# Optimization experiments

Hardware: AMD Instinct MI355X
Metric: run time of the kernel (lower is better)

## Reference

```python
import jax, jax.numpy as jnp
import numpy as np

NEG_SLOPE = 0.01  # F.leaky_relu default
EPS = 1e-6


def setup_inputs() -> dict:
    key = jax.random.key(0)
    k1, k2, k3, k4 = jax.random.split(key, 4)
    N, E, IN, OUT = 100000, 1600000, 128, 64
    x = jax.random.normal(k1, (N, IN), dtype=jnp.float32)
    W = jax.random.normal(k2, (OUT, IN), dtype=jnp.float32) * (1.0 / np.sqrt(IN))
    a = jax.random.uniform(k3, (2 * OUT,), dtype=jnp.float32)  # uniform [0,1) as in init
    edge_index = jax.random.randint(k4, (2, E), 0, N, dtype=jnp.int64)
    return {"x": x, "W": W, "a": a, "edge_index": edge_index}


def reference(x, W, a, edge_index):
    N = x.shape[0]
    out_f = W.shape[0]
    # add self loops: append (i, i) for every node
    loops = jnp.arange(N, dtype=edge_index.dtype)
    ei = jnp.concatenate([edge_index, jnp.stack([loops, loops])], axis=1)
    src, dst = ei[0], ei[1]

    messages = x @ W.T                      # [N, out]
    h_src = messages[src]                   # [E', out]
    h_dst = messages[dst]                   # [E', out]

    # e = cat([h_dst, h_src]) . a  == h_dst.a[:out] + h_src.a[out:]
    e = h_dst @ a[:out_f] + h_src @ a[out_f:]
    e = jnp.where(e >= 0, e, NEG_SLOPE * e)  # leaky_relu
    w = jnp.exp(e)                           # unnormalized edge weights

    denom = jax.ops.segment_sum(w, dst, num_segments=N)                     # [N]
    agg = jax.ops.segment_sum(h_src * w[:, None], dst, num_segments=N)      # [N, out]
    return agg / jnp.clip(denom, EPS)[:, None]
```

## Files before the change

### kernel.cpp

```cpp
#include <hip/hip_runtime.h>
#include <hip/hip_bf16.h>

#define IN_F 128
#define OUT_F 64
#define NEG 0.01f

#define BUCKET_N 256
#define EPB 8192
#define CAP 48
#define MAXB 512
#define MAXSLAB 512
#define CMAXIT 32

__device__ __forceinline__ float leaky_exp(float e) {
    e = (e >= 0.f) ? e : NEG * e;
    return expf(e);
}

__device__ __forceinline__ float b2f(unsigned int v) { return __uint_as_float(v); }

__global__ __launch_bounds__(256) void wt_kernel(
    const float* __restrict__ W, float* __restrict__ Wtg)
{
    int i = blockIdx.x * 256 + threadIdx.x;
    int o = i >> 7, k = i & 127;
    Wtg[k * OUT_F + o] = W[i];
}

__global__ __launch_bounds__(256) void gemm_msg_kernel(
    const float* __restrict__ x, const float* __restrict__ Wtg,
    const float* __restrict__ a,
    __hip_bfloat16* __restrict__ msg, float2* __restrict__ ab, int N)
{
    const int tid = threadIdx.x;
    const int base = blockIdx.x * 64;
    const int tx = tid & 15;
    const int ty = tid >> 4;

    const float4* xr[4];
#pragma unroll
    for (int ri = 0; ri < 4; ++ri) {
        int row = min(base + ty * 4 + ri, N - 1);
        xr[ri] = (const float4*)x + (size_t)row * (IN_F / 4);
    }

    float4 xc[4];
#pragma unroll
    for (int ri = 0; ri < 4; ++ri) xc[ri] = xr[ri][0];

    const float4* wt4 = (const float4*)Wtg;

    float acc[4][4] = {};
#pragma unroll 2
    for (int k4 = 0; k4 < IN_F / 4; ++k4) {
        float4 xn[4];
        const int kn = min(k4 + 1, IN_F / 4 - 1);
#pragma unroll
        for (int ri = 0; ri < 4; ++ri) xn[ri] = xr[ri][kn];

        float wq[4][4];
#pragma unroll
        for (int j = 0; j < 4; ++j)
            *(float4*)wq[j] = wt4[(k4 * 4 + j) * (OUT_F / 4) + tx];
        float xq[4][4];
#pragma unroll
        for (int ri = 0; ri < 4; ++ri) *(float4*)xq[ri] = xc[ri];

#pragma unroll
        for (int ri = 0; ri < 4; ++ri)
#pragma unroll
            for (int ci = 0; ci < 4; ++ci) {
                acc[ri][ci] += xq[ri][0] * wq[0][ci];
                acc[ri][ci] += xq[ri][1] * wq[1][ci];
                acc[ri][ci] += xq[ri][2] * wq[2][ci];
                acc[ri][ci] += xq[ri][3] * wq[3][ci];
            }
#pragma unroll
        for (int ri = 0; ri < 4; ++ri) xc[ri] = xn[ri];
    }

    float a_lo[4], a_hi[4];
#pragma unroll
    for (int ci = 0; ci < 4; ++ci) {
        a_lo[ci] = a[tx * 4 + ci];
        a_hi[ci] = a[OUT_F + tx * 4 + ci];
    }

#pragma unroll
    for (int ri = 0; ri < 4; ++ri) {
        int row = base + ty * 4 + ri;
        if (row < N) {
            union { ushort4 u; __hip_bfloat16 h[4]; } pk;
            pk.h[0] = __float2bfloat16(acc[ri][0]);
            pk.h[1] = __float2bfloat16(acc[ri][1]);
            pk.h[2] = __float2bfloat16(acc[ri][2]);
            pk.h[3] = __float2bfloat16(acc[ri][3]);
            *(ushort4*)&msg[(size_t)row * OUT_F + tx * 4] = pk.u;
        }
        float pa = acc[ri][0] * a_lo[0] + acc[ri][1] * a_lo[1] +
                   acc[ri][2] * a_lo[2] + acc[ri][3] * a_lo[3];
        float pb = acc[ri][0] * a_hi[0] + acc[ri][1] * a_hi[1] +
                   acc[ri][2] * a_hi[2] + acc[ri][3] * a_hi[3];
#pragma unroll
        for (int off = 1; off < 16; off <<= 1) {
            pa += __shfl_xor(pa, off);
            pb += __shfl_xor(pb, off);
        }
        if (tx == 0 && row < N) ab[row] = make_float2(pa, pb);
    }
}

__global__ __launch_bounds__(512) void partition_kernel(
    const int* __restrict__ src, const int* __restrict__ dst,
    int* __restrict__ counts, unsigned int* __restrict__ cells,
    int* __restrict__ bucket_tot, int E, int B, int NBLKP)
{
    __shared__ int cnt_s[MAXB];
    for (int i = threadIdx.x; i < B; i += 512) cnt_s[i] = 0;
    __syncthreads();

    const size_t pbase = (size_t)blockIdx.x * B;

#pragma unroll
    for (int u = 0; u < 4; ++u) {
        const int i4 = blockIdx.x * 2048 + u * 512 + threadIdx.x;
        const int e0 = i4 * 4;
        if (e0 + 3 < E) {
            int4 s4 = ((const int4*)src)[i4];
            int4 d4 = ((const int4*)dst)[i4];
            int b0 = d4.x >> 8, b1 = d4.y >> 8, b2 = d4.z >> 8, b3 = d4.w >> 8;
            int r0 = atomicAdd(&cnt_s[b0], 1);
            int r1 = atomicAdd(&cnt_s[b1], 1);
            int r2 = atomicAdd(&cnt_s[b2], 1);
            int r3 = atomicAdd(&cnt_s[b3], 1);
            if (r0 < CAP) cells[(pbase + b0) * CAP + r0] =
                (unsigned)s4.x | ((unsigned)(d4.x & 255) << 20);
            if (r1 < CAP) cells[(pbase + b1) * CAP + r1] =
                (unsigned)s4.y | ((unsigned)(d4.y & 255) << 20);
            if (r2 < CAP) cells[(pbase + b2) * CAP + r2] =
                (unsigned)s4.z | ((unsigned)(d4.z & 255) << 20);
            if (r3 < CAP) cells[(pbase + b3) * CAP + r3] =
                (unsigned)s4.w | ((unsigned)(d4.w & 255) << 20);
        } else {
            for (int e = e0; e < E && e < e0 + 4; ++e) {
                int s = src[e], d = dst[e];
                int b = d >> 8;
                int r = atomicAdd(&cnt_s[b], 1);
                if (r < CAP) cells[(pbase + b) * CAP + r] =
                    (unsigned)s | ((unsigned)(d & 255) << 20);
            }
        }
    }
    __syncthreads();
    for (int i = threadIdx.x; i < B; i += 512) {
        int c = min(cnt_s[i], CAP);
        counts[(size_t)i * NBLKP + blockIdx.x] = c;
        atomicAdd(&bucket_tot[i], c);
    }
}

__global__ __launch_bounds__(512) void bucket_scan_kernel(
    const int* __restrict__ bucket_tot, int* __restrict__ bucket_base,
    int* __restrict__ offs, int N, int B)
{
    __shared__ int tmp[512];
    const int t = threadIdx.x;
    int v = 0;
    if (t < B) {
        int nodes = N - t * BUCKET_N;
        nodes = max(0, min(BUCKET_N, nodes));
        v = bucket_tot[t] + nodes;
    }
    tmp[t] = v;
    __syncthreads();
#pragma unroll
    for (int d = 1; d < 512; d <<= 1) {
        int add = (t >= d) ? tmp[t - d] : 0;
        __syncthreads();
        tmp[t] += add;
        __syncthreads();
    }
    if (t < B) bucket_base[t] = tmp[t] - v;
    if (t == 511) offs[N] = tmp[511];
}

__global__ __launch_bounds__(512) void compact_kernel(
    const int* __restrict__ counts, const unsigned int* __restrict__ cells,
    const int* __restrict__ bucket_base, const float2* __restrict__ ab,
    int* __restrict__ offs, int2* __restrict__ edges,
    int N, int B, int NBLK, int NBLKP)
{
    __shared__ int cnt_l[MAXSLAB];
    __shared__ int hist[BUCKET_N];
    __shared__ int scan_s[BUCKET_N];
    __shared__ int cursor[BUCKET_N];
    __shared__ float alpha_s[BUCKET_N];
    const int b = blockIdx.x;
    const int tid = threadIdx.x;
    const int wave = tid >> 6, lane = tid & 63;

    for (int i = tid; i < NBLK; i += 512) cnt_l[i] = counts[(size_t)b * NBLKP + i];
    float2 myab = make_float2(0.f, 0.f);
    if (tid < BUCKET_N) {
        int g = b * BUCKET_N + tid;
        bool valid = (g < N);
        hist[tid] = valid ? 1 : 0;
        if (valid) myab = ab[g];
        alpha_s[tid] = myab.x;
    }
    __syncthreads();

    unsigned cell_c[CMAXIT];
#pragma unroll
    for (int it = 0; it < CMAXIT; ++it) {
        int sl = wave + it * 8;
        unsigned v = 0xFFFFFFFFu;
        if (sl < NBLK) {
            int c = cnt_l[sl];
            if (lane < c) {
                v = cells[((size_t)sl * B + b) * CAP + lane];
                atomicAdd(&hist[v >> 20], 1);
            }
        }
        cell_c[it] = v;
    }
    for (int sl = wave + CMAXIT * 8; sl < NBLK; sl += 8) {
        int c = cnt_l[sl];
        if (lane < c) {
            unsigned v = cells[((size_t)sl * B + b) * CAP + lane];
            atomicAdd(&hist[v >> 20], 1);
        }
    }
    __syncthreads();

    int hv = 0;
    if (tid < BUCKET_N) { hv = hist[tid]; scan_s[tid] = hv; }
    __syncthreads();
#pragma unroll
    for (int d = 1; d < BUCKET_N; d <<= 1) {
        int add = (tid < BUCKET_N && tid >= d) ? scan_s[tid - d] : 0;
        __syncthreads();
        if (tid < BUCKET_N) scan_s[tid] += add;
        __syncthreads();
    }
    const int gbase = bucket_base[b];
    if (tid < BUCKET_N) {
        int excl = scan_s[tid] - hv;
        int g = b * BUCKET_N + tid;
        if (g < N) {
            offs[g] = gbase + excl;
            float wself = leaky_exp(myab.x + myab.y);
            edges[gbase + excl] = make_int2(g, __float_as_int(wself));
            cursor[tid] = excl + 1;
        }
    }
    __syncthreads();

#pragma unroll
    for (int it = 0; it < CMAXIT; ++it) {
        unsigned v = cell_c[it];
        if (v != 0xFFFFFFFFu) {
            int s = v & 0xFFFFF;
            int l = (v >> 20) & 255;
            float w = leaky_exp(alpha_s[l] + ab[s].y);
            int pos = atomicAdd(&cursor[l], 1);
            edges[gbase + pos] = make_int2(s, __float_as_int(w));
        }
    }
    for (int sl = wave + CMAXIT * 8; sl < NBLK; sl += 8) {
        int c = cnt_l[sl];
        if (lane < c) {
            unsigned v = cells[((size_t)sl * B + b) * CAP + lane];
            int s = v & 0xFFFFF;
            int l = (v >> 20) & 255;
            float w = leaky_exp(alpha_s[l] + ab[s].y);
            int pos = atomicAdd(&cursor[l], 1);
            edges[gbase + pos] = make_int2(s, __float_as_int(w));
        }
    }
}

__global__ __launch_bounds__(256) void aggregate_kernel(
    const int* __restrict__ offs, const int2* __restrict__ edges,
    const __hip_bfloat16* __restrict__ msg,
    float* __restrict__ out, int N)
{
    const int tid = threadIdx.x;
    const int node = blockIdx.x * 8 + (tid >> 5);
    if (node >= N) return;
    const int half = tid & 31;
    const int g = half & 7;
    const int u = half >> 3;

    const unsigned int* msp32 = (const unsigned int*)msg;

    float acc[8] = {0.f, 0.f, 0.f, 0.f, 0.f, 0.f, 0.f, 0.f};
    float den = 0.f;

    const int st = offs[node], en = offs[node + 1];
    const int deg = en - st;

    int idx = st + u;
    int j = 0;
    for (; j + 16 <= deg; j += 16) {
#pragma unroll
        for (int q = 0; q < 4; ++q) {
            int2 e = edges[idx + q * 4];
            float w = __int_as_float(e.y);
            uint4 m = *(const uint4*)&msp32[(size_t)e.x * (OUT_F / 2) + 4 * g];
            acc[0] += w * b2f(m.x << 16);
            acc[1] += w * b2f(m.x & 0xFFFF0000u);
            acc[2] += w * b2f(m.y << 16);
            acc[3] += w * b2f(m.y & 0xFFFF0000u);
            acc[4] += w * b2f(m.z << 16);
            acc[5] += w * b2f(m.z & 0xFFFF0000u);
            acc[6] += w * b2f(m.w << 16);
            acc[7] += w * b2f(m.w & 0xFFFF0000u);
            den += w;
        }
        idx += 16;
    }
    for (; j < deg; j += 4) {
        int ii = min(idx, en - 1);
        int2 e = edges[ii];
        float w = (idx < en) ? __int_as_float(e.y) : 0.f;
        uint4 m = *(const uint4*)&msp32[(size_t)e.x * (OUT_F / 2) + 4 * g];
        acc[0] += w * b2f(m.x << 16);
        acc[1] += w * b2f(m.x & 0xFFFF0000u);
        acc[2] += w * b2f(m.y << 16);
        acc[3] += w * b2f(m.y & 0xFFFF0000u);
        acc[4] += w * b2f(m.z << 16);
        acc[5] += w * b2f(m.z & 0xFFFF0000u);
        acc[6] += w * b2f(m.w << 16);
        acc[7] += w * b2f(m.w & 0xFFFF0000u);
        den += w;
        idx += 4;
    }

#pragma unroll
    for (int off = 8; off <= 16; off <<= 1) {
#pragma unroll
        for (int i = 0; i < 8; ++i) acc[i] += __shfl_xor(acc[i], off);
        den += __shfl_xor(den, off);
    }

    if (u == 0) {
        float dn = 1.f / fmaxf(den, 1e-6f);
        float4* op = (float4*)&out[(size_t)node * OUT_F + 8 * g];
        op[0] = make_float4(acc[0] * dn, acc[1] * dn, acc[2] * dn, acc[3] * dn);
        op[1] = make_float4(acc[4] * dn, acc[5] * dn, acc[6] * dn, acc[7] * dn);
    }
}

extern "C" void kernel_launch(void* const* d_in, const int* in_sizes, int n_in,
                              void* d_out, int out_size, void* d_ws, size_t ws_size,
                              hipStream_t stream) {
    const float* x  = (const float*)d_in[0];
    const float* W  = (const float*)d_in[1];
    const float* a  = (const float*)d_in[2];
    const int*   ei = (const int*)d_in[3];
    float* out = (float*)d_out;

    const int IN = in_sizes[1] / OUT_F;
    const int N  = in_sizes[0] / IN;
    const int E  = in_sizes[3] / 2;
    const int B  = (N + BUCKET_N - 1) / BUCKET_N;
    const int NBLK  = (E + EPB - 1) / EPB;
    const int NBLKP = (NBLK + 3) & ~3;

    auto align16 = [](size_t v) { return (v + 15) & ~(size_t)15; };
    char* p = (char*)d_ws;
    float* Wtg    = (float*)p; p += align16((size_t)IN_F * OUT_F * 4);
    __hip_bfloat16* msg = (__hip_bfloat16*)p; p += align16((size_t)N * OUT_F * 2);
    float2* ab    = (float2*)p; p += align16((size_t)N * 8);
    int*   counts = (int*)p;   p += align16((size_t)B * NBLKP * 4);
    unsigned int* cells = (unsigned int*)p; p += align16((size_t)NBLK * B * CAP * 4);
    int*   btot   = (int*)p;   p += align16((size_t)B * 4);
    int*   bbase  = (int*)p;   p += align16((size_t)B * 4);
    int*   offs   = (int*)p;   p += align16((size_t)(N + 1) * 4);
    int2*  edges  = (int2*)p;  p += align16((size_t)(E + N) * 8);

    const int* esrc = ei;
    const int* edst = ei + E;

    hipMemsetAsync(btot, 0, (size_t)B * 4, stream);

    wt_kernel<<<(IN_F * OUT_F) / 256, 256, 0, stream>>>(W, Wtg);
    gemm_msg_kernel<<<(N + 63) / 64, 256, 0, stream>>>(x, Wtg, a, msg, ab, N);
    partition_kernel<<<NBLK, 512, 0, stream>>>(esrc, edst, counts, cells,
                                               btot, E, B, NBLKP);
    bucket_scan_kernel<<<1, 512, 0, stream>>>(btot, bbase, offs, N, B);
    compact_kernel<<<B, 512, 0, stream>>>(counts, cells, bbase, ab,
                                          offs, edges, N, B, NBLK, NBLKP);
    aggregate_kernel<<<(N + 7) / 8, 256, 0, stream>>>(offs, edges, msg, out, N);
}
```

Measured before the change: 152.7 us.

## Hold W rows in registers, process one node per wave in GEMM

The GEMM is rewritten so that each lane keeps one full row of W (128 floats) in registers. Each wave then walks a contiguous range of nodes, and every lane produces one output feature per node. The x row is loaded uniformly across the wave, so it acts as a broadcast load. The attention dot products are now reduced with a 64-lane shuffle. The separate W transpose kernel and its workspace are removed. The cost is heavy register pressure (over 128 VGPRs per lane), which lowers occupancy, and a fixed grid of 1024 blocks with about 25 rows per wave.

After: 226.9 us. +48.6%, slower.

```diff
diff --git a/kernel.cpp b/kernel.cpp
--- a/kernel.cpp
+++ b/kernel.cpp
@@ -19,94 +19,63 @@
 
 __device__ __forceinline__ float b2f(unsigned int v) { return __uint_as_float(v); }
 
-__global__ __launch_bounds__(256) void wt_kernel(
-    const float* __restrict__ W, float* __restrict__ Wtg)
-{
-    int i = blockIdx.x * 256 + threadIdx.x;
-    int o = i >> 7, k = i & 127;
-    Wtg[k * OUT_F + o] = W[i];
-}
-
 __global__ __launch_bounds__(256) void gemm_msg_kernel(
-    const float* __restrict__ x, const float* __restrict__ Wtg,
+    const float* __restrict__ x, const float* __restrict__ W,
     const float* __restrict__ a,
-    __hip_bfloat16* __restrict__ msg, float2* __restrict__ ab, int N)
-{
-    const int tid = threadIdx.x;
-    const int base = blockIdx.x * 64;
-    const int tx = tid & 15;
-    const int ty = tid >> 4;
-
-    const float4* xr[4];
-#pragma unroll
-    for (int ri = 0; ri < 4; ++ri) {
-        int row = min(base + ty * 4 + ri, N - 1);
-        xr[ri] = (const float4*)x + (size_t)row * (IN_F / 4);
-    }
-
-    float4 xc[4];
-#pragma unroll
-    for (int ri = 0; ri < 4; ++ri) xc[ri] = xr[ri][0];
-
-    const float4* wt4 = (const float4*)Wtg;
-
-    float acc[4][4] = {};
-#pragma unroll 2
+    __hip_bfloat16* __restrict__ msg, float2* __restrict__ ab,
+    int N, int nwaves)
+{
+    const int lane = threadIdx.x & 63;
+
+    float w[IN_F];
+    const float4* wrow = (const float4*)(W + (size_t)lane * IN_F);
+#pragma unroll
     for (int k4 = 0; k4 < IN_F / 4; ++k4) {
-        float4 xn[4];
-        const int kn = min(k4 + 1, IN_F / 4 - 1);
-#pragma unroll
-        for (int ri = 0; ri < 4; ++ri) xn[ri] = xr[ri][kn];
-
-        float wq[4][4];
-#pragma unroll
-        for (int j = 0; j < 4; ++j)
-            *(float4*)wq[j] = wt4[(k4 * 4 + j) * (OUT_F / 4) + tx];
-        float xq[4][4];
-#pragma unroll
-        for (int ri = 0; ri < 4; ++ri) *(float4*)xq[ri] = xc[ri];
-
-#pragma unroll
-        for (int ri = 0; ri < 4; ++ri)
-#pragma unroll
-            for (int ci = 0; ci < 4; ++ci) {
-                acc[ri][ci] += xq[ri][0] * wq[0][ci];
-                acc[ri][ci] += xq[ri][1] * wq[1][ci];
-                acc[ri][ci] += xq[ri][2] * wq[2][ci];
-                acc[ri][ci] += xq[ri][3] * wq[3][ci];
-            }
-#pragma unroll
-        for (int ri = 0; ri < 4; ++ri) xc[ri] = xn[ri];
-    }
-
-    float a_lo[4], a_hi[4];
-#pragma unroll
-    for (int ci = 0; ci < 4; ++ci) {
-        a_lo[ci] = a[tx * 4 + ci];
-        a_hi[ci] = a[OUT_F + tx * 4 + ci];
-    }
-
-#pragma unroll
-    for (int ri = 0; ri < 4; ++ri) {
-        int row = base + ty * 4 + ri;
-        if (row < N) {
-            union { ushort4 u; __hip_bfloat16 h[4]; } pk;
-            pk.h[0] = __float2bfloat16(acc[ri][0]);
-            pk.h[1] = __float2bfloat16(acc[ri][1]);
-            pk.h[2] = __float2bfloat16(acc[ri][2]);
-            pk.h[3] = __float2bfloat16(acc[ri][3]);
-            *(ushort4*)&msg[(size_t)row * OUT_F + tx * 4] = pk.u;
-        }
-        float pa = acc[ri][0] * a_lo[0] + acc[ri][1] * a_lo[1] +
-                   acc[ri][2] * a_lo[2] + acc[ri][3] * a_lo[3];
-        float pb = acc[ri][0] * a_hi[0] + acc[ri][1] * a_hi[1] +
-                   acc[ri][2] * a_hi[2] + acc[ri][3] * a_hi[3];
-#pragma unroll
-        for (int off = 1; off < 16; off <<= 1) {
+        float4 wv = wrow[k4];
+        w[4 * k4 + 0] = wv.x;
+        w[4 * k4 + 1] = wv.y;
+        w[4 * k4 + 2] = wv.z;
+        w[4 * k4 + 3] = wv.w;
+    }
+    const float a_lo = a[lane];
+    const float a_hi = a[OUT_F + lane];
+
+    const int wid = __builtin_amdgcn_readfirstlane(
+        blockIdx.x * (blockDim.x >> 6) + (threadIdx.x >> 6));
+    const int rpw = (N + nwaves - 1) / nwaves;
+    const int r0 = wid * rpw;
+    const int r1 = min(r0 + rpw, N);
+
+    for (int row = r0; row < r1; ++row) {
+        const float4* xrow = (const float4*)(x + (size_t)row * IN_F);
+        float av0 = 0.f, av1 = 0.f, av2 = 0.f, av3 = 0.f;
+#pragma unroll
+        for (int k4 = 0; k4 < IN_F / 4; k4 += 4) {
+            float4 x0 = xrow[k4 + 0];
+            float4 x1 = xrow[k4 + 1];
+            float4 x2 = xrow[k4 + 2];
+            float4 x3 = xrow[k4 + 3];
+            av0 += x0.x * w[4 * k4 + 0] + x0.y * w[4 * k4 + 1]
+                 + x0.z * w[4 * k4 + 2] + x0.w * w[4 * k4 + 3];
+            av1 += x1.x * w[4 * k4 + 4] + x1.y * w[4 * k4 + 5]
+                 + x1.z * w[4 * k4 + 6] + x1.w * w[4 * k4 + 7];
+            av2 += x2.x * w[4 * k4 + 8] + x2.y * w[4 * k4 + 9]
+                 + x2.z * w[4 * k4 + 10] + x2.w * w[4 * k4 + 11];
+            av3 += x3.x * w[4 * k4 + 12] + x3.y * w[4 * k4 + 13]
+                 + x3.z * w[4 * k4 + 14] + x3.w * w[4 * k4 + 15];
+        }
+        const float acc = (av0 + av1) + (av2 + av3);
+
+        msg[(size_t)row * OUT_F + lane] = __float2bfloat16(acc);
+
+        float pa = acc * a_lo;
+        float pb = acc * a_hi;
+#pragma unroll
+        for (int off = 1; off < 64; off <<= 1) {
             pa += __shfl_xor(pa, off);
             pb += __shfl_xor(pb, off);
         }
-        if (tx == 0 && row < N) ab[row] = make_float2(pa, pb);
+        if (lane == 0) ab[row] = make_float2(pa, pb);
     }
 }
 
@@ -370,7 +339,6 @@
 
     auto align16 = [](size_t v) { return (v + 15) & ~(size_t)15; };
     char* p = (char*)d_ws;
-    float* Wtg    = (float*)p; p += align16((size_t)IN_F * OUT_F * 4);
     __hip_bfloat16* msg = (__hip_bfloat16*)p; p += align16((size_t)N * OUT_F * 2);
     float2* ab    = (float2*)p; p += align16((size_t)N * 8);
     int*   counts = (int*)p;   p += align16((size_t)B * NBLKP * 4);
@@ -385,8 +353,9 @@
 
     hipMemsetAsync(btot, 0, (size_t)B * 4, stream);
 
-    wt_kernel<<<(IN_F * OUT_F) / 256, 256, 0, stream>>>(W, Wtg);
-    gemm_msg_kernel<<<(N + 63) / 64, 256, 0, stream>>>(x, Wtg, a, msg, ab, N);
+    const int gemm_blocks = 1024;
+    const int nwaves = gemm_blocks * 4;
+    gemm_msg_kernel<<<gemm_blocks, 256, 0, stream>>>(x, W, a, msg, ab, N, nwaves);
     partition_kernel<<<NBLK, 512, 0, stream>>>(esrc, edst, counts, cells,
                                                btot, E, B, NBLKP);
     bucket_scan_kernel<<<1, 512, 0, stream>>>(btot, bbase, offs, N, B);
```
